# Performance work log

Measured on AMD Instinct MI355X. Metric: run time of the kernel, lower is better.

## Reference

```python
import jax, jax.numpy as jnp
import numpy as np
import math

WIN = (3, 3, 3)
DIL = 1
B, N, C = 2, 8192, 128
D = H = W = 48


def _offsets():
    # same ordering as torch get_offset_coord: row-major over (win0,win1,win2)
    half = [math.ceil(w * 0.5) - 1 for w in WIN]
    axes = [jnp.arange(-half[i], WIN[i] - half[i]) for i in range(3)]
    g = jnp.stack(jnp.meshgrid(*axes, indexing='ij'), axis=-1).reshape(-1, 3)  # (K,3)
    # dilation applies to the first two spatial dims (D,H)
    return g * jnp.array([DIL, DIL, 1], dtype=g.dtype)


def setup_inputs() -> dict:
    key = jax.random.key(0)
    ks = jax.random.split(key, 10)
    s = 1.0 / np.sqrt(C)
    return {
        'q_feat': jax.random.normal(ks[0], (B, N, C), jnp.float32),
        'feat': jax.random.normal(ks[1], (B, C, D, H, W), jnp.float32),
        'proj_coord': jax.random.randint(ks[2], (B, N, 3), 0, 48, jnp.int32),
        'hr_coord': jax.random.uniform(ks[3], (B, N, 3), jnp.float32),
        'q_w': jax.random.normal(ks[4], (C, C), jnp.float32) * s,
        'q_b': jax.random.normal(ks[5], (C,), jnp.float32) * s,
        'k_w': jax.random.normal(ks[6], (C, C), jnp.float32) * s,
        'k_b': jax.random.normal(ks[7], (C,), jnp.float32) * s,
        'v_w': jax.random.normal(ks[8], (C, C), jnp.float32) * s,
        'v_b': jax.random.normal(ks[9], (C,), jnp.float32) * s,
    }


def reference(q_feat, feat, proj_coord, hr_coord, q_w, q_b, k_w, k_b, v_w, v_b):
    b, c = feat.shape[:2]
    n = proj_coord.shape[1]
    off = _offsets()                                  # (K,3)
    K = off.shape[0]
    p = [WIN[0] // 2 * DIL, WIN[1] // 2 * DIL, WIN[2] // 2]
    # replication padding (torch ReplicationPad3d == edge mode)
    padded = jnp.pad(feat, ((0, 0), (0, 0), (p[0], p[0]), (p[1], p[1]), (p[2], p[2])), mode='edge')
    Dp, Hp, Wp = padded.shape[2:]
    # absolute window coords in padded volume: (b,N,K,3)
    coords = proj_coord[:, :, None, :] + jnp.array(p, jnp.int32) + off.astype(jnp.int32)
    flat = coords[..., 0] * (Hp * Wp) + coords[..., 1] * Wp + coords[..., 2]  # (b,N,K)
    feat_flat = padded.reshape(b, c, -1).transpose(0, 2, 1)                   # (b,S,c)
    local_feat = jnp.take_along_axis(feat_flat, flat.reshape(b, -1, 1), axis=1)
    local_feat = local_feat.reshape(b, n, K, c)
    # FBLA: q/k attention over local window
    q = q_feat @ q_w.T + q_b                          # (b,N,c)
    k = jnp.einsum('bnkc,dc->bnkd', local_feat, k_w) + k_b
    atten = jax.nn.softmax(jnp.einsum('bnd,bnkd->bnk', q, k), axis=-1)
    v = jnp.einsum('bnkc,dc->bnkd', local_feat, v_w) + v_b
    x = jnp.einsum('bnk,bnkd->bnd', atten, v)
    return q_feat + x
```

## Files before the change

kernel.cpp:

```cpp
#include <hip/hip_runtime.h>
#include <cstdint>

typedef unsigned short u16;
typedef unsigned int   u32;

__device__ __forceinline__ float bf2f(u16 u){ return __uint_as_float(((u32)u) << 16); }
__device__ __forceinline__ float bflo(u32 u){ return __uint_as_float(u << 16); }
__device__ __forceinline__ float bfhi(u32 u){ return __uint_as_float(u & 0xffff0000u); }
__device__ __forceinline__ u16 f2bf(float f){
    u32 x = __float_as_uint(f);
    u32 r = x + 0x7fffu + ((x >> 16) & 1u);
    return (u16)(r >> 16);
}
__device__ __forceinline__ int detect_bf16(const void* p){
    const u16* h = (const u16*)p;
    int hits = 0;
    for (int i = 0; i < 64; ++i){
        const int e = (h[2 * i] >> 7) & 0xFF;
        hits += (e >= 110 && e <= 140) ? 1 : 0;
    }
    return hits >= 40;
}
__device__ __forceinline__ int detect_i64(const int* p){
    int z = 0;
    for (int i = 0; i < 48; ++i) z += (p[2 * i + 1] == 0) ? 1 : 0;
    return z >= 40;
}
__device__ __forceinline__ float ldf(const void* p, size_t i, int isbf){
    return isbf ? bf2f(((const u16*)p)[i]) : ((const float*)p)[i];
}
__device__ __forceinline__ void read_proj(const int* proj, int q, int p64,
                                          int& pz, int& py, int& px){
    if (p64){
        pz = proj[(size_t)(q * 3 + 0) * 2];
        py = proj[(size_t)(q * 3 + 1) * 2];
        px = proj[(size_t)(q * 3 + 2) * 2];
    } else {
        pz = proj[q * 3 + 0]; py = proj[q * 3 + 1]; px = proj[q * 3 + 2];
    }
    pz = min(max(pz, 0), 47); py = min(max(py, 0), 47); px = min(max(px, 0), 47);
}

__global__ __launch_bounds__(128) void k_prep(const void* __restrict__ qw_,
                                              const void* __restrict__ qb_,
                                              const void* __restrict__ kw_,
                                              float* __restrict__ M, float* __restrict__ bias){
    const int e = blockIdx.x, c = threadIdx.x;
    const int is_qw = detect_bf16(qw_), is_kw = detect_bf16(kw_), is_qb = detect_bf16(qb_);
    float acc = 0.f;
    for (int d = 0; d < 128; ++d)
        acc += ldf(kw_, (size_t)d * 128 + c, is_kw) * ldf(qw_, (size_t)d * 128 + e, is_qw);
    M[e * 128 + c] = acc;
    if (e == 0){
        float ab = 0.f;
        for (int d = 0; d < 128; ++d)
            ab += ldf(kw_, (size_t)d * 128 + c, is_kw) * ldf(qb_, d, is_qb);
        bias[c] = ab;
    }
}

__global__ __launch_bounds__(256) void k_w2(const void* __restrict__ vw_, float* __restrict__ W2){
    const int i = blockIdx.x * 256 + threadIdx.x;
    const int c = i >> 7, d = i & 127;
    const int is_vw = detect_bf16(vw_);
    W2[c * 128 + d] = ldf(vw_, (size_t)d * 128 + c, is_vw);
}

__global__ __launch_bounds__(256) void k_tr(const void* __restrict__ feat_,
                                            u16* __restrict__ featT){
    __shared__ u32 sh[4096];
    __shared__ int sbf;
    const int t = threadIdx.x;
    if (t == 0) sbf = detect_bf16(feat_);
    __syncthreads();
    const int isbf = sbf;
    const int chunk = blockIdx.x;
    const int b = chunk / 1728;
    const size_t rel = (size_t)(chunk - b * 1728) * 64;
    if (isbf){
        const u16* f = (const u16*)feat_;
        for (int it = 0; it < 4; ++it){
            const int i = it * 256 + t;
            const int c2 = i >> 4, q16 = i & 15;
            const size_t sA = ((size_t)(b * 128 + 2 * c2    )) * 110592 + rel + q16 * 4;
            const size_t sB = ((size_t)(b * 128 + 2 * c2 + 1)) * 110592 + rel + q16 * 4;
            const uint2 va = *reinterpret_cast<const uint2*>(f + sA);
            const uint2 vb = *reinterpret_cast<const uint2*>(f + sB);
            const u32 vals[4] = {
                (va.x & 0xffffu) | (vb.x << 16),
                (va.x >> 16)     | (vb.x & 0xffff0000u),
                (va.y & 0xffffu) | (vb.y << 16),
                (va.y >> 16)     | (vb.y & 0xffff0000u)
            };
#pragma unroll
            for (int j = 0; j < 4; ++j){
                const int v = q16 * 4 + j;
                const int xv = (v ^ (v >> 4)) & 15;
                sh[v * 64 + (c2 & 3) + 4 * ((c2 >> 2) ^ xv)] = vals[j];
            }
        }
    } else {
        const float* f = (const float*)feat_;
        for (int it = 0; it < 4; ++it){
            const int i = it * 256 + t;
            const int c2 = i >> 4, q16 = i & 15;
            const size_t sA = ((size_t)(b * 128 + 2 * c2    )) * 110592 + rel + q16 * 4;
            const size_t sB = ((size_t)(b * 128 + 2 * c2 + 1)) * 110592 + rel + q16 * 4;
            const float4 a  = *reinterpret_cast<const float4*>(f + sA);
            const float4 bv = *reinterpret_cast<const float4*>(f + sB);
            const float av[4] = {a.x, a.y, a.z, a.w};
            const float bw[4] = {bv.x, bv.y, bv.z, bv.w};
#pragma unroll
            for (int j = 0; j < 4; ++j){
                const int v = q16 * 4 + j;
                const int xv = (v ^ (v >> 4)) & 15;
                sh[v * 64 + (c2 & 3) + 4 * ((c2 >> 2) ^ xv)] =
                    (u32)f2bf(av[j]) | ((u32)f2bf(bw[j]) << 16);
            }
        }
    }
    __syncthreads();
    u32* ft = reinterpret_cast<u32*>(featT);
    const size_t obase = (size_t)chunk * 4096;
#pragma unroll
    for (int k = 0; k < 4; ++k){
        const int G = k * 256 + t;
        const int v = G >> 4, gr = G & 15;
        const int xv = (v ^ (v >> 4)) & 15;
        const uint4 val = *reinterpret_cast<const uint4*>(&sh[v * 64 + 4 * (gr ^ xv)]);
        *reinterpret_cast<uint4*>(ft + obase + (size_t)G * 4) = val;
    }
}

__global__ __launch_bounds__(256) void k_qk(const void* __restrict__ qf_,
                                            const float* __restrict__ M,
                                            const float* __restrict__ bias,
                                            float* __restrict__ qk_all){
    __shared__ float Msh[128 * 128];
    const int t = threadIdx.x;
    const int is_qf = detect_bf16(qf_);
    {
        const float4* Mg4 = reinterpret_cast<const float4*>(M);
        float4* Ms4 = reinterpret_cast<float4*>(Msh);
        for (int i = t; i < 4096; i += 256) Ms4[i] = Mg4[i];
    }
    __syncthreads();
    const int tg = t >> 5, lane32 = t & 31;
    const int cq = lane32 * 4;
    const float4 b4 = *reinterpret_cast<const float4*>(bias + cq);
    const int qbase = blockIdx.x * 32;
    for (int qi = tg; qi < 32; qi += 16){
        const int qa = qbase + qi, qb2 = qbase + qi + 8;
        float qvA[4], qvB[4];
        if (is_qf){
            const ushort4 a = *reinterpret_cast<const ushort4*>((const u16*)qf_ + (size_t)qa * 128 + lane32 * 4);
            const ushort4 b = *reinterpret_cast<const ushort4*>((const u16*)qf_ + (size_t)qb2 * 128 + lane32 * 4);
            qvA[0]=bf2f(a.x); qvA[1]=bf2f(a.y); qvA[2]=bf2f(a.z); qvA[3]=bf2f(a.w);
            qvB[0]=bf2f(b.x); qvB[1]=bf2f(b.y); qvB[2]=bf2f(b.z); qvB[3]=bf2f(b.w);
        } else {
            const float4 a = *reinterpret_cast<const float4*>((const float*)qf_ + (size_t)qa * 128 + lane32 * 4);
            const float4 b = *reinterpret_cast<const float4*>((const float*)qf_ + (size_t)qb2 * 128 + lane32 * 4);
            qvA[0]=a.x; qvA[1]=a.y; qvA[2]=a.z; qvA[3]=a.w;
            qvB[0]=b.x; qvB[1]=b.y; qvB[2]=b.z; qvB[3]=b.w;
        }
        float4 accA = b4, accB = b4;
#pragma unroll 4
        for (int es = 0; es < 32; ++es){
#pragma unroll
            for (int j = 0; j < 4; ++j){
                const int e = es * 4 + j;
                const float4 m = *reinterpret_cast<const float4*>(&Msh[e * 128 + cq]);
                const float qeA = __shfl(qvA[j], es, 32);
                const float qeB = __shfl(qvB[j], es, 32);
                accA.x += qeA * m.x; accA.y += qeA * m.y; accA.z += qeA * m.z; accA.w += qeA * m.w;
                accB.x += qeB * m.x; accB.y += qeB * m.y; accB.z += qeB * m.z; accB.w += qeB * m.w;
            }
        }
        *reinterpret_cast<float4*>(qk_all + (size_t)qa  * 128 + cq) = accA;
        *reinterpret_cast<float4*>(qk_all + (size_t)qb2 * 128 + cq) = accB;
    }
}

__global__ __launch_bounds__(256) void k_attn_feat(const u16* __restrict__ featT,
                                                   const float* __restrict__ qk_all,
                                                   const int* __restrict__ proj,
                                                   float* __restrict__ g){
    const int lane = threadIdx.x & 63;
    const int q = blockIdx.x * 4 + (threadIdx.x >> 6);
    const int kg = lane >> 4, cl = lane & 15;
    const int b = q >> 13;
    const int p64 = detect_i64(proj);
    int pz, py, px; read_proj(proj, q, p64, pz, py, px);
    const float4* qp4 = reinterpret_cast<const float4*>(qk_all + (size_t)q * 128 + cl * 8);
    const float4 qA = qp4[0], qB = qp4[1];
    const u16* base = featT + (size_t)b * 14155776 + cl * 8;
    uint4 fr[7];
    float sc[7];
#pragma unroll
    for (int s = 0; s < 7; ++s){
        const int k = s * 4 + kg;
        uint4 v = make_uint4(0u, 0u, 0u, 0u);
        if (k < 27){
            const int dz = k / 9, r9 = k - dz * 9, dy = r9 / 3, dx = r9 - dy * 3;
            const int zz = min(max(pz - 1 + dz, 0), 47);
            const int yy = min(max(py - 1 + dy, 0), 47);
            const int xx = min(max(px - 1 + dx, 0), 47);
            v = *reinterpret_cast<const uint4*>(base + (size_t)(zz * 2304 + yy * 48 + xx) * 128);
        }
        fr[s] = v;
        float t = qA.x * bflo(v.x) + qA.y * bfhi(v.x)
                + qA.z * bflo(v.y) + qA.w * bfhi(v.y)
                + qB.x * bflo(v.z) + qB.y * bfhi(v.z)
                + qB.z * bflo(v.w) + qB.w * bfhi(v.w);
        t += __shfl_xor(t, 1, 64);
        t += __shfl_xor(t, 2, 64);
        t += __shfl_xor(t, 4, 64);
        t += __shfl_xor(t, 8, 64);
        sc[s] = (k < 27) ? t : -1e30f;
    }
    float mx = sc[0];
#pragma unroll
    for (int s = 1; s < 7; ++s) mx = fmaxf(mx, sc[s]);
    mx = fmaxf(mx, __shfl_xor(mx, 16, 64));
    mx = fmaxf(mx, __shfl_xor(mx, 32, 64));
    float e[7], Z = 0.f;
#pragma unroll
    for (int s = 0; s < 7; ++s){ e[s] = __expf(sc[s] - mx); Z += e[s]; }
    Z += __shfl_xor(Z, 16, 64);
    Z += __shfl_xor(Z, 32, 64);
    const float inv = 1.0f / Z;
    float w[8];
#pragma unroll
    for (int i = 0; i < 8; ++i) w[i] = 0.f;
#pragma unroll
    for (int s = 0; s < 7; ++s){
        const float a = e[s] * inv;
        w[0] += a * bflo(fr[s].x); w[1] += a * bfhi(fr[s].x);
        w[2] += a * bflo(fr[s].y); w[3] += a * bfhi(fr[s].y);
        w[4] += a * bflo(fr[s].z); w[5] += a * bfhi(fr[s].z);
        w[6] += a * bflo(fr[s].w); w[7] += a * bfhi(fr[s].w);
    }
#pragma unroll
    for (int i = 0; i < 8; ++i){
        w[i] += __shfl_xor(w[i], 16, 64);
        w[i] += __shfl_xor(w[i], 32, 64);
    }
    if (kg == 0){
        float4 lo4; lo4.x = w[0]; lo4.y = w[1]; lo4.z = w[2]; lo4.w = w[3];
        float4 hi4; hi4.x = w[4]; hi4.y = w[5]; hi4.z = w[6]; hi4.w = w[7];
        float4* o = reinterpret_cast<float4*>(g + (size_t)q * 128 + cl * 8);
        o[0] = lo4; o[1] = hi4;
    }
}

__global__ __launch_bounds__(256) void k_attn_direct(const void* __restrict__ feat_,
                                                     const float* __restrict__ qk_all,
                                                     const int* __restrict__ proj,
                                                     float* __restrict__ g){
    const int lane = threadIdx.x & 63;
    const int q = blockIdx.x * 4 + (threadIdx.x >> 6);
    const int kg = lane >> 4, cl = lane & 15;
    const int b = q >> 13;
    const int isbf = detect_bf16(feat_);
    const int p64 = detect_i64(proj);
    int pz, py, px; read_proj(proj, q, p64, pz, py, px);
    const float* qk = qk_all + (size_t)q * 128 + cl * 8;
    float qv[8];
#pragma unroll
    for (int i = 0; i < 8; ++i) qv[i] = qk[i];
    const size_t cbase = ((size_t)b * 128 + cl * 8) * 110592;
    float f[7][8];
    float sc[7];
#pragma unroll
    for (int s = 0; s < 7; ++s){
        const int k = s * 4 + kg;
#pragma unroll
        for (int i = 0; i < 8; ++i) f[s][i] = 0.f;
        if (k < 27){
            const int dz = k / 9, r9 = k - dz * 9, dy = r9 / 3, dx = r9 - dy * 3;
            const int zz = min(max(pz - 1 + dz, 0), 47);
            const int yy = min(max(py - 1 + dy, 0), 47);
            const int xx = min(max(px - 1 + dx, 0), 47);
            const size_t off = (size_t)zz * 2304 + yy * 48 + xx;
#pragma unroll
            for (int i = 0; i < 8; ++i) f[s][i] = ldf(feat_, cbase + (size_t)i * 110592 + off, isbf);
        }
        float t = 0.f;
#pragma unroll
        for (int i = 0; i < 8; ++i) t += qv[i] * f[s][i];
        t += __shfl_xor(t, 1, 64);
        t += __shfl_xor(t, 2, 64);
        t += __shfl_xor(t, 4, 64);
        t += __shfl_xor(t, 8, 64);
        sc[s] = (k < 27) ? t : -1e30f;
    }
    float mx = sc[0];
#pragma unroll
    for (int s = 1; s < 7; ++s) mx = fmaxf(mx, sc[s]);
    mx = fmaxf(mx, __shfl_xor(mx, 16, 64));
    mx = fmaxf(mx, __shfl_xor(mx, 32, 64));
    float e[7], Z = 0.f;
#pragma unroll
    for (int s = 0; s < 7; ++s){ e[s] = __expf(sc[s] - mx); Z += e[s]; }
    Z += __shfl_xor(Z, 16, 64);
    Z += __shfl_xor(Z, 32, 64);
    const float inv = 1.0f / Z;
    float w[8];
#pragma unroll
    for (int i = 0; i < 8; ++i) w[i] = 0.f;
#pragma unroll
    for (int s = 0; s < 7; ++s){
        const float a = e[s] * inv;
#pragma unroll
        for (int i = 0; i < 8; ++i) w[i] += a * f[s][i];
    }
#pragma unroll
    for (int i = 0; i < 8; ++i){
        w[i] += __shfl_xor(w[i], 16, 64);
        w[i] += __shfl_xor(w[i], 32, 64);
    }
    if (kg == 0){
        float4 lo4; lo4.x = w[0]; lo4.y = w[1]; lo4.z = w[2]; lo4.w = w[3];
        float4 hi4; hi4.x = w[4]; hi4.y = w[5]; hi4.z = w[6]; hi4.w = w[7];
        float4* o = reinterpret_cast<float4*>(g + (size_t)q * 128 + cl * 8);
        o[0] = lo4; o[1] = hi4;
    }
}

__global__ __launch_bounds__(256) void k_out(const float* __restrict__ g,
                                             const float* __restrict__ W2,
                                             const void* __restrict__ qf_,
                                             const void* __restrict__ vb_,
                                             float* __restrict__ out){
    __shared__ float Wsh[128 * 128];
    const int t = threadIdx.x;
    const int is_qf = detect_bf16(qf_);
    const int is_vb = detect_bf16(vb_);
    {
        const float4* Wg4 = reinterpret_cast<const float4*>(W2);
        float4* Ws4 = reinterpret_cast<float4*>(Wsh);
        for (int i = t; i < 4096; i += 256) Ws4[i] = Wg4[i];
    }
    __syncthreads();
    const int tg = t >> 5, lane32 = t & 31;
    const int dq = lane32 * 4;
    float4 vb4;
    if (is_vb){
        const ushort4 v = *reinterpret_cast<const ushort4*>((const u16*)vb_ + dq);
        vb4.x = bf2f(v.x); vb4.y = bf2f(v.y); vb4.z = bf2f(v.z); vb4.w = bf2f(v.w);
    } else {
        vb4 = *reinterpret_cast<const float4*>((const float*)vb_ + dq);
    }
    const int qbase = blockIdx.x * 32;
    for (int qi = tg; qi < 32; qi += 16){
        const int qa = qbase + qi, qb2 = qbase + qi + 8;
        const float4 gA = *reinterpret_cast<const float4*>(g + (size_t)qa  * 128 + lane32 * 4);
        const float4 gB = *reinterpret_cast<const float4*>(g + (size_t)qb2 * 128 + lane32 * 4);
        const float gvA[4] = {gA.x, gA.y, gA.z, gA.w};
        const float gvB[4] = {gB.x, gB.y, gB.z, gB.w};
        float4 accA = vb4, accB = vb4;
#pragma unroll 4
        for (int cs = 0; cs < 32; ++cs){
#pragma unroll
            for (int j = 0; j < 4; ++j){
                const int c = cs * 4 + j;
                const float4 m = *reinterpret_cast<const float4*>(&Wsh[c * 128 + dq]);
                const float geA = __shfl(gvA[j], cs, 32);
                const float geB = __shfl(gvB[j], cs, 32);
                accA.x += geA * m.x; accA.y += geA * m.y; accA.z += geA * m.z; accA.w += geA * m.w;
                accB.x += geB * m.x; accB.y += geB * m.y; accB.z += geB * m.z; accB.w += geB * m.w;
            }
        }
        float4 rA, rB;
        if (is_qf){
            const ushort4 a = *reinterpret_cast<const ushort4*>((const u16*)qf_ + (size_t)qa * 128 + dq);
            const ushort4 b = *reinterpret_cast<const ushort4*>((const u16*)qf_ + (size_t)qb2 * 128 + dq);
            rA.x = bf2f(a.x); rA.y = bf2f(a.y); rA.z = bf2f(a.z); rA.w = bf2f(a.w);
            rB.x = bf2f(b.x); rB.y = bf2f(b.y); rB.z = bf2f(b.z); rB.w = bf2f(b.w);
        } else {
            rA = *reinterpret_cast<const float4*>((const float*)qf_ + (size_t)qa * 128 + dq);
            rB = *reinterpret_cast<const float4*>((const float*)qf_ + (size_t)qb2 * 128 + dq);
        }
        accA.x += rA.x; accA.y += rA.y; accA.z += rA.z; accA.w += rA.w;
        accB.x += rB.x; accB.y += rB.y; accB.z += rB.z; accB.w += rB.w;
        *reinterpret_cast<float4*>(out + (size_t)qa  * 128 + dq) = accA;
        *reinterpret_cast<float4*>(out + (size_t)qb2 * 128 + dq) = accB;
    }
}

__global__ __launch_bounds__(128) void k_simple(const void* __restrict__ qf_,
                                                const void* __restrict__ feat_,
                                                const void* __restrict__ proj_,
                                                const void* __restrict__ qw_,
                                                const void* __restrict__ qb_,
                                                const void* __restrict__ kw_,
                                                const void* __restrict__ kb_,
                                                const void* __restrict__ vw_,
                                                const void* __restrict__ vb_,
                                                float* __restrict__ out){
    __shared__ float qfs[128];
    __shared__ float qs[128];
    __shared__ float ts[128];
    __shared__ float gs[128];
    __shared__ float ss4[27][4];
    __shared__ float aa[27];
    __shared__ float kbd[1];
    const int t = threadIdx.x;
    const int q = blockIdx.x;
    const int b = q >> 13;
    const int is_qf = detect_bf16(qf_);
    const int is_ft = detect_bf16(feat_);
    const int is_qw = detect_bf16(qw_);
    const int is_qb = detect_bf16(qb_);
    const int is_kw = detect_bf16(kw_);
    const int is_kb = detect_bf16(kb_);
    const int is_vw = detect_bf16(vw_);
    const int is_vb = detect_bf16(vb_);
    const int p64   = detect_i64((const int*)proj_);
    qfs[t] = ldf(qf_, (size_t)q * 128 + t, is_qf);
    __syncthreads();
    {
        float acc = ldf(qb_, t, is_qb);
        for (int e = 0; e < 128; ++e)
            acc += ldf(qw_, (size_t)t * 128 + e, is_qw) * qfs[e];
        qs[t] = acc;
    }
    __syncthreads();
    {
        float acc = 0.f;
        for (int d = 0; d < 128; ++d)
            acc += ldf(kw_, (size_t)d * 128 + t, is_kw) * qs[d];
        ts[t] = acc;
    }
    if (t == 0){
        float kd = 0.f;
        for (int d = 0; d < 128; ++d) kd += ldf(kb_, d, is_kb) * qs[d];
        kbd[0] = kd;
    }
    __syncthreads();
    int pz, py, px; read_proj((const int*)proj_, q, p64, pz, py, px);
    if (t < 108){
        const int k = t >> 2, part = t & 3;
        const int dz = k / 9, dy = (k / 3) % 3, dx = k % 3;
        const int zz = min(max(pz - 1 + dz, 0), 47);
        const int yy = min(max(py - 1 + dy, 0), 47);
        const int xx = min(max(px - 1 + dx, 0), 47);
        const size_t sp = (size_t)zz * 2304 + yy * 48 + xx;
        float s = 0.f;
        for (int c = part * 32; c < part * 32 + 32; ++c)
            s += ts[c] * ldf(feat_, ((size_t)b * 128 + c) * 110592 + sp, is_ft);
        ss4[k][part] = s;
    }
    __syncthreads();
    if (t == 0){
        float sc[27];
        float mx = -1e30f;
        for (int k = 0; k < 27; ++k){
            sc[k] = ss4[k][0] + ss4[k][1] + ss4[k][2] + ss4[k][3] + kbd[0];
            mx = fmaxf(mx, sc[k]);
        }
        float Z = 0.f;
        for (int k = 0; k < 27; ++k){ sc[k] = expf(sc[k] - mx); Z += sc[k]; }
        const float inv = 1.0f / Z;
        for (int k = 0; k < 27; ++k) aa[k] = sc[k] * inv;
    }
    __syncthreads();
    {
        float g = 0.f;
        const size_t cb = ((size_t)b * 128 + t) * 110592;
        for (int k = 0; k < 27; ++k){
            const int dz = k / 9, dy = (k / 3) % 3, dx = k % 3;
            const int zz = min(max(pz - 1 + dz, 0), 47);
            const int yy = min(max(py - 1 + dy, 0), 47);
            const int xx = min(max(px - 1 + dx, 0), 47);
            g += aa[k] * ldf(feat_, cb + (size_t)zz * 2304 + yy * 48 + xx, is_ft);
        }
        gs[t] = g;
    }
    __syncthreads();
    {
        float o = qfs[t] + ldf(vb_, t, is_vb);
        for (int c = 0; c < 128; ++c)
            o += ldf(vw_, (size_t)t * 128 + c, is_vw) * gs[c];
        out[(size_t)q * 128 + t] = o;
    }
}

extern "C" void kernel_launch(void* const* d_in, const int* in_sizes, int n_in,
                              void* d_out, int out_size, void* d_ws, size_t ws_size,
                              hipStream_t stream) {
    const void* qfeat = d_in[0];
    const void* feat  = d_in[1];
    const int*  proj  = (const int*)d_in[2];
    const void* qw = d_in[4];
    const void* qb = d_in[5];
    const void* kw = d_in[6];
    const void* kb = d_in[7];
    const void* vw = d_in[8];
    const void* vb = d_in[9];
    float* out = (float*)d_out;

    char* wsb = (char*)d_ws;
    float* M      = (float*)(wsb);
    float* bias   = (float*)(wsb + 65536);
    float* W2     = (float*)(wsb + 66048);
    float* qk_all = (float*)(wsb + 131584);
    float* g      = (float*)(wsb + 8520192);
    u16*   featT  = (u16*)  (wsb + 16908800);

    const int tier = (ws_size >= (size_t)73531904) ? 1
                   : (ws_size >= (size_t)16908800) ? 2 : 3;

    if (tier == 3){
        hipLaunchKernelGGL(k_simple, dim3(16384), dim3(128), 0, stream,
                           qfeat, feat, proj, qw, qb, kw, kb, vw, vb, out);
        return;
    }
    hipLaunchKernelGGL(k_prep, dim3(128), dim3(128), 0, stream, qw, qb, kw, M, bias);
    hipLaunchKernelGGL(k_w2,   dim3(64),  dim3(256), 0, stream, vw, W2);
    hipLaunchKernelGGL(k_qk,   dim3(512), dim3(256), 0, stream, qfeat, M, bias, qk_all);
    if (tier == 1){
        hipLaunchKernelGGL(k_tr,        dim3(3456), dim3(256), 0, stream, feat, featT);
        hipLaunchKernelGGL(k_attn_feat, dim3(4096), dim3(256), 0, stream, featT, qk_all, proj, g);
    } else {
        hipLaunchKernelGGL(k_attn_direct, dim3(4096), dim3(256), 0, stream, feat, qk_all, proj, g);
    }
    hipLaunchKernelGGL(k_out,  dim3(512), dim3(256), 0, stream, g, W2, qfeat, vb, out);
}
```

Before: 332.7 us.

## Register-tile k_qk and k_out GEMMs and merge prep kernels into one launch

The small 128x128 GEMMs in k_qk and k_out now stage a transposed tile of 32 query rows in shared memory. Each thread computes a 4x4 register tile, replacing the earlier shuffle-based broadcast that handled 2 rows at a time. This cuts LDS and shuffle traffic per FMA. The separate k_w2 transpose kernel is folded into k_prep, removing one launch. It costs extra shared memory (16 KB per block) and more registers per thread.

```diff
diff --git a/kernel.cpp b/kernel.cpp
--- a/kernel.cpp
+++ b/kernel.cpp
@@ -41,29 +41,34 @@
     pz = min(max(pz, 0), 47); py = min(max(py, 0), 47); px = min(max(px, 0), 47);
 }
 
-__global__ __launch_bounds__(128) void k_prep(const void* __restrict__ qw_,
+__global__ __launch_bounds__(256) void k_prep(const void* __restrict__ qw_,
                                               const void* __restrict__ qb_,
                                               const void* __restrict__ kw_,
-                                              float* __restrict__ M, float* __restrict__ bias){
-    const int e = blockIdx.x, c = threadIdx.x;
-    const int is_qw = detect_bf16(qw_), is_kw = detect_bf16(kw_), is_qb = detect_bf16(qb_);
-    float acc = 0.f;
-    for (int d = 0; d < 128; ++d)
-        acc += ldf(kw_, (size_t)d * 128 + c, is_kw) * ldf(qw_, (size_t)d * 128 + e, is_qw);
-    M[e * 128 + c] = acc;
-    if (e == 0){
-        float ab = 0.f;
+                                              const void* __restrict__ vw_,
+                                              float* __restrict__ M,
+                                              float* __restrict__ bias,
+                                              float* __restrict__ W2){
+    const int bid = blockIdx.x, t = threadIdx.x;
+    if (bid < 64){
+        const int e = bid * 2 + (t >> 7), c = t & 127;
+        const int is_qw = detect_bf16(qw_), is_kw = detect_bf16(kw_);
+        float acc = 0.f;
         for (int d = 0; d < 128; ++d)
-            ab += ldf(kw_, (size_t)d * 128 + c, is_kw) * ldf(qb_, d, is_qb);
-        bias[c] = ab;
-    }
-}
-
-__global__ __launch_bounds__(256) void k_w2(const void* __restrict__ vw_, float* __restrict__ W2){
-    const int i = blockIdx.x * 256 + threadIdx.x;
-    const int c = i >> 7, d = i & 127;
-    const int is_vw = detect_bf16(vw_);
-    W2[c * 128 + d] = ldf(vw_, (size_t)d * 128 + c, is_vw);
+            acc += ldf(kw_, (size_t)d * 128 + c, is_kw) * ldf(qw_, (size_t)d * 128 + e, is_qw);
+        M[e * 128 + c] = acc;
+        if (bid == 0 && t < 128){
+            const int is_qb = detect_bf16(qb_);
+            float ab = 0.f;
+            for (int d = 0; d < 128; ++d)
+                ab += ldf(kw_, (size_t)d * 128 + t, is_kw) * ldf(qb_, d, is_qb);
+            bias[t] = ab;
+        }
+    } else {
+        const int i = (bid - 64) * 256 + t;
+        const int c = i >> 7, d = i & 127;
+        const int is_vw = detect_bf16(vw_);
+        W2[c * 128 + d] = ldf(vw_, (size_t)d * 128 + c, is_vw);
+    }
 }
 
 __global__ __launch_bounds__(256) void k_tr(const void* __restrict__ feat_,
@@ -137,48 +142,52 @@
                                             const float* __restrict__ bias,
                                             float* __restrict__ qk_all){
     __shared__ float Msh[128 * 128];
+    __shared__ float qT[128 * 32];
     const int t = threadIdx.x;
     const int is_qf = detect_bf16(qf_);
+    const int qbase = blockIdx.x * 32;
     {
         const float4* Mg4 = reinterpret_cast<const float4*>(M);
         float4* Ms4 = reinterpret_cast<float4*>(Msh);
         for (int i = t; i < 4096; i += 256) Ms4[i] = Mg4[i];
     }
-    __syncthreads();
-    const int tg = t >> 5, lane32 = t & 31;
-    const int cq = lane32 * 4;
-    const float4 b4 = *reinterpret_cast<const float4*>(bias + cq);
-    const int qbase = blockIdx.x * 32;
-    for (int qi = tg; qi < 32; qi += 16){
-        const int qa = qbase + qi, qb2 = qbase + qi + 8;
-        float qvA[4], qvB[4];
+#pragma unroll
+    for (int p = 0; p < 4; ++p){
+        const int i = p * 256 + t;
+        const int q = i & 31, gr = i >> 5;
+        float v[4];
         if (is_qf){
-            const ushort4 a = *reinterpret_cast<const ushort4*>((const u16*)qf_ + (size_t)qa * 128 + lane32 * 4);
-            const ushort4 b = *reinterpret_cast<const ushort4*>((const u16*)qf_ + (size_t)qb2 * 128 + lane32 * 4);
-            qvA[0]=bf2f(a.x); qvA[1]=bf2f(a.y); qvA[2]=bf2f(a.z); qvA[3]=bf2f(a.w);
-            qvB[0]=bf2f(b.x); qvB[1]=bf2f(b.y); qvB[2]=bf2f(b.z); qvB[3]=bf2f(b.w);
+            const ushort4 a = *reinterpret_cast<const ushort4*>((const u16*)qf_ + (size_t)(qbase + q) * 128 + gr * 4);
+            v[0] = bf2f(a.x); v[1] = bf2f(a.y); v[2] = bf2f(a.z); v[3] = bf2f(a.w);
         } else {
-            const float4 a = *reinterpret_cast<const float4*>((const float*)qf_ + (size_t)qa * 128 + lane32 * 4);
-            const float4 b = *reinterpret_cast<const float4*>((const float*)qf_ + (size_t)qb2 * 128 + lane32 * 4);
-            qvA[0]=a.x; qvA[1]=a.y; qvA[2]=a.z; qvA[3]=a.w;
-            qvB[0]=b.x; qvB[1]=b.y; qvB[2]=b.z; qvB[3]=b.w;
-        }
-        float4 accA = b4, accB = b4;
+            const float4 a = *reinterpret_cast<const float4*>((const float*)qf_ + (size_t)(qbase + q) * 128 + gr * 4);
+            v[0] = a.x; v[1] = a.y; v[2] = a.z; v[3] = a.w;
+        }
+#pragma unroll
+        for (int j = 0; j < 4; ++j) qT[(gr * 4 + j) * 32 + q] = v[j];
+    }
+    __syncthreads();
+    const int g  = t & 31;
+    const int qa = t >> 5;
+    const float4 b4 = *reinterpret_cast<const float4*>(bias + g * 4);
+    float4 acc0 = b4, acc1 = b4, acc2 = b4, acc3 = b4;
 #pragma unroll 4
-        for (int es = 0; es < 32; ++es){
-#pragma unroll
-            for (int j = 0; j < 4; ++j){
-                const int e = es * 4 + j;
-                const float4 m = *reinterpret_cast<const float4*>(&Msh[e * 128 + cq]);
-                const float qeA = __shfl(qvA[j], es, 32);
-                const float qeB = __shfl(qvB[j], es, 32);
-                accA.x += qeA * m.x; accA.y += qeA * m.y; accA.z += qeA * m.z; accA.w += qeA * m.w;
-                accB.x += qeB * m.x; accB.y += qeB * m.y; accB.z += qeB * m.z; accB.w += qeB * m.w;
-            }
-        }
-        *reinterpret_cast<float4*>(qk_all + (size_t)qa  * 128 + cq) = accA;
-        *reinterpret_cast<float4*>(qk_all + (size_t)qb2 * 128 + cq) = accB;
-    }
+    for (int e = 0; e < 128; ++e){
+        const float4 qv = *reinterpret_cast<const float4*>(&qT[e * 32 + qa * 4]);
+        const float4 m  = *reinterpret_cast<const float4*>(&Msh[e * 128 + g * 4]);
+        acc0.x += qv.x * m.x; acc0.y += qv.x * m.y; acc0.z += qv.x * m.z; acc0.w += qv.x * m.w;
+        acc1.x += qv.y * m.x; acc1.y += qv.y * m.y; acc1.z += qv.y * m.z; acc1.w += qv.y * m.w;
+        acc2.x += qv.z * m.x; acc2.y += qv.z * m.y; acc2.z += qv.z * m.z; acc2.w += qv.z * m.w;
+        acc3.x += qv.w * m.x; acc3.y += qv.w * m.y; acc3.z += qv.w * m.z; acc3.w += qv.w * m.w;
+    }
+    float* o0 = qk_all + (size_t)(qbase + qa * 4 + 0) * 128 + g * 4;
+    float* o1 = qk_all + (size_t)(qbase + qa * 4 + 1) * 128 + g * 4;
+    float* o2 = qk_all + (size_t)(qbase + qa * 4 + 2) * 128 + g * 4;
+    float* o3 = qk_all + (size_t)(qbase + qa * 4 + 3) * 128 + g * 4;
+    *reinterpret_cast<float4*>(o0) = acc0;
+    *reinterpret_cast<float4*>(o1) = acc1;
+    *reinterpret_cast<float4*>(o2) = acc2;
+    *reinterpret_cast<float4*>(o3) = acc3;
 }
 
 __global__ __launch_bounds__(256) void k_attn_feat(const u16* __restrict__ featT,
@@ -327,64 +336,65 @@
     }
 }
 
-__global__ __launch_bounds__(256) void k_out(const float* __restrict__ g,
+__global__ __launch_bounds__(256) void k_out(const float* __restrict__ gbuf,
                                              const float* __restrict__ W2,
                                              const void* __restrict__ qf_,
                                              const void* __restrict__ vb_,
                                              float* __restrict__ out){
     __shared__ float Wsh[128 * 128];
+    __shared__ float gT[128 * 32];
     const int t = threadIdx.x;
     const int is_qf = detect_bf16(qf_);
     const int is_vb = detect_bf16(vb_);
+    const int qbase = blockIdx.x * 32;
     {
         const float4* Wg4 = reinterpret_cast<const float4*>(W2);
         float4* Ws4 = reinterpret_cast<float4*>(Wsh);
         for (int i = t; i < 4096; i += 256) Ws4[i] = Wg4[i];
     }
-    __syncthreads();
-    const int tg = t >> 5, lane32 = t & 31;
-    const int dq = lane32 * 4;
+#pragma unroll
+    for (int p = 0; p < 4; ++p){
+        const int i = p * 256 + t;
+        const int q = i & 31, gr = i >> 5;
+        const float4 a = *reinterpret_cast<const float4*>(gbuf + (size_t)(qbase + q) * 128 + gr * 4);
+        gT[(gr * 4 + 0) * 32 + q] = a.x;
+        gT[(gr * 4 + 1) * 32 + q] = a.y;
+        gT[(gr * 4 + 2) * 32 + q] = a.z;
+        gT[(gr * 4 + 3) * 32 + q] = a.w;
+    }
+    __syncthreads();
+    const int g  = t & 31;
+    const int qa = t >> 5;
     float4 vb4;
     if (is_vb){
-        const ushort4 v = *reinterpret_cast<const ushort4*>((const u16*)vb_ + dq);
+        const ushort4 v = *reinterpret_cast<const ushort4*>((const u16*)vb_ + g * 4);
         vb4.x = bf2f(v.x); vb4.y = bf2f(v.y); vb4.z = bf2f(v.z); vb4.w = bf2f(v.w);
     } else {
-        vb4 = *reinterpret_cast<const float4*>((const float*)vb_ + dq);
-    }
-    const int qbase = blockIdx.x * 32;
-    for (int qi = tg; qi < 32; qi += 16){
-        const int qa = qbase + qi, qb2 = qbase + qi + 8;
-        const float4 gA = *reinterpret_cast<const float4*>(g + (size_t)qa  * 128 + lane32 * 4);
-        const float4 gB = *reinterpret_cast<const float4*>(g + (size_t)qb2 * 128 + lane32 * 4);
-        const float gvA[4] = {gA.x, gA.y, gA.z, gA.w};
-        const float gvB[4] = {gB.x, gB.y, gB.z, gB.w};
-        float4 accA = vb4, accB = vb4;
+        vb4 = *reinterpret_cast<const float4*>((const float*)vb_ + g * 4);
+    }
+    float4 acc0 = vb4, acc1 = vb4, acc2 = vb4, acc3 = vb4;
 #pragma unroll 4
-        for (int cs = 0; cs < 32; ++cs){
-#pragma unroll
-            for (int j = 0; j < 4; ++j){
-                const int c = cs * 4 + j;
-                const float4 m = *reinterpret_cast<const float4*>(&Wsh[c * 128 + dq]);
-                const float geA = __shfl(gvA[j], cs, 32);
-                const float geB = __shfl(gvB[j], cs, 32);
-                accA.x += geA * m.x; accA.y += geA * m.y; accA.z += geA * m.z; accA.w += geA * m.w;
-                accB.x += geB * m.x; accB.y += geB * m.y; accB.z += geB * m.z; accB.w += geB * m.w;
-            }
-        }
-        float4 rA, rB;
+    for (int c = 0; c < 128; ++c){
+        const float4 gv = *reinterpret_cast<const float4*>(&gT[c * 32 + qa * 4]);
+        const float4 m  = *reinterpret_cast<const float4*>(&Wsh[c * 128 + g * 4]);
+        acc0.x += gv.x * m.x; acc0.y += gv.x * m.y; acc0.z += gv.x * m.z; acc0.w += gv.x * m.w;
+        acc1.x += gv.y * m.x; acc1.y += gv.y * m.y; acc1.z += gv.y * m.z; acc1.w += gv.y * m.w;
+        acc2.x += gv.z * m.x; acc2.y += gv.z * m.y; acc2.z += gv.z * m.z; acc2.w += gv.z * m.w;
+        acc3.x += gv.w * m.x; acc3.y += gv.w * m.y; acc3.z += gv.w * m.z; acc3.w += gv.w * m.w;
+    }
+#pragma unroll
+    for (int j = 0; j < 4; ++j){
+        const int q = qbase + qa * 4 + j;
+        float4 acc = (j == 0) ? acc0 : (j == 1) ? acc1 : (j == 2) ? acc2 : acc3;
+        float4 r;
         if (is_qf){
-            const ushort4 a = *reinterpret_cast<const ushort4*>((const u16*)qf_ + (size_t)qa * 128 + dq);
-            const ushort4 b = *reinterpret_cast<const ushort4*>((const u16*)qf_ + (size_t)qb2 * 128 + dq);
-            rA.x = bf2f(a.x); rA.y = bf2f(a.y); rA.z = bf2f(a.z); rA.w = bf2f(a.w);
-            rB.x = bf2f(b.x); rB.y = bf2f(b.y); rB.z = bf2f(b.z); rB.w = bf2f(b.w);
+            const ushort4 a = *reinterpret_cast<const ushort4*>((const u16*)qf_ + (size_t)q * 128 + g * 4);
+            r.x = bf2f(a.x); r.y = bf2f(a.y); r.z = bf2f(a.z); r.w = bf2f(a.w);
         } else {
-            rA = *reinterpret_cast<const float4*>((const float*)qf_ + (size_t)qa * 128 + dq);
-            rB = *reinterpret_cast<const float4*>((const float*)qf_ + (size_t)qb2 * 128 + dq);
-        }
-        accA.x += rA.x; accA.y += rA.y; accA.z += rA.z; accA.w += rA.w;
-        accB.x += rB.x; accB.y += rB.y; accB.z += rB.z; accB.w += rB.w;
-        *reinterpret_cast<float4*>(out + (size_t)qa  * 128 + dq) = accA;
-        *reinterpret_cast<float4*>(out + (size_t)qb2 * 128 + dq) = accB;
+            r = *reinterpret_cast<const float4*>((const float*)qf_ + (size_t)q * 128 + g * 4);
+        }
+        acc.x += r.x; acc.y += r.y; acc.z += r.z; acc.w += r.w;
+        *reinterpret_cast<float4*>(out + (size_t)q * 128 + g * 4) = acc;
     }
 }
 
@@ -516,8 +526,7 @@
                            qfeat, feat, proj, qw, qb, kw, kb, vw, vb, out);
         return;
     }
-    hipLaunchKernelGGL(k_prep, dim3(128), dim3(128), 0, stream, qw, qb, kw, M, bias);
-    hipLaunchKernelGGL(k_w2,   dim3(64),  dim3(256), 0, stream, vw, W2);
+    hipLaunchKernelGGL(k_prep, dim3(128), dim3(256), 0, stream, qw, qb, kw, vw, M, bias, W2);
     hipLaunchKernelGGL(k_qk,   dim3(512), dim3(256), 0, stream, qfeat, M, bias, qk_all);
     if (tier == 1){
         hipLaunchKernelGGL(k_tr,        dim3(3456), dim3(256), 0, stream, feat, featT);
```

After: 295.6 us. -11.1%, faster.
